# Performance work log

Hardware: AMD Instinct MI355X
Metric: run time of the kernel (lower is better)

## Reference

```python
import jax, jax.numpy as jnp
import numpy as np

P, F, V = 2048, 8192, 2048


def setup_inputs() -> dict:
    key = jax.random.key(0)
    k1, k2, k3 = jax.random.split(key, 3)
    points = jax.random.normal(k1, (P, 3), dtype=jnp.float32)
    vertices = jax.random.normal(k2, (V, 3), dtype=jnp.float32)
    faces = jax.random.randint(k3, (F, 3), 0, V, dtype=jnp.int32)
    return {"points": points, "vertices": vertices, "faces": faces}


def _triangle_weights(points, a, b, c):
    """Barycentric weights of closest point on each triangle (a,b,c) [F,3]
    for each point [P,3], via Ericson's region classification.
    All pairwise dot products expanded so only [P,F] scalars are materialized
    (never [P,F,3] differences)."""
    ab = b - a  # [F,3]
    ac = c - a  # [F,3]
    pab = points @ ab.T  # [P,F] = dot(p, ab)
    pac = points @ ac.T  # [P,F] = dot(p, ac)
    d1 = pab - jnp.sum(a * ab, -1)  # dot(ab, p-a)
    d2 = pac - jnp.sum(a * ac, -1)  # dot(ac, p-a)
    d3 = pab - jnp.sum(b * ab, -1)  # dot(ab, p-b)
    d4 = pac - jnp.sum(b * ac, -1)  # dot(ac, p-b)
    d5 = pab - jnp.sum(c * ab, -1)  # dot(ab, p-c)
    d6 = pac - jnp.sum(c * ac, -1)  # dot(ac, p-c)
    vc = d1 * d4 - d3 * d2
    vb = d5 * d2 - d1 * d6
    va = d3 * d6 - d5 * d4

    def sdiv(n, d):
        ds = jnp.where(d == 0, 1.0, d)
        return n / ds

    # region 7 (interior) is the default; overwrite with higher-priority
    denom = va + vb + vc
    v7 = sdiv(vb, denom)
    w7 = sdiv(vc, denom)
    w1, w2, w3 = 1.0 - v7 - w7, v7, w7
    # region 6: edge bc
    t6 = sdiv(d4 - d3, (d4 - d3) + (d5 - d6))
    m6 = (va <= 0) & (d4 - d3 >= 0) & (d5 - d6 >= 0)
    w1 = jnp.where(m6, 0.0, w1)
    w2 = jnp.where(m6, 1.0 - t6, w2)
    w3 = jnp.where(m6, t6, w3)
    # region 5: edge ac
    t5 = sdiv(d2, d2 - d6)
    m5 = (vb <= 0) & (d2 >= 0) & (d6 <= 0)
    w1 = jnp.where(m5, 1.0 - t5, w1)
    w2 = jnp.where(m5, 0.0, w2)
    w3 = jnp.where(m5, t5, w3)
    # region 4: vertex c
    m4 = (d6 >= 0) & (d5 <= d6)
    w1 = jnp.where(m4, 0.0, w1)
    w2 = jnp.where(m4, 0.0, w2)
    w3 = jnp.where(m4, 1.0, w3)
    # region 3: edge ab
    t3 = sdiv(d1, d1 - d3)
    m3 = (vc <= 0) & (d1 >= 0) & (d3 <= 0)
    w1 = jnp.where(m3, 1.0 - t3, w1)
    w2 = jnp.where(m3, t3, w2)
    w3 = jnp.where(m3, 0.0, w3)
    # region 2: vertex b
    m2 = (d3 >= 0) & (d4 <= d3)
    w1 = jnp.where(m2, 0.0, w1)
    w2 = jnp.where(m2, 1.0, w2)
    w3 = jnp.where(m2, 0.0, w3)
    # region 1: vertex a
    m1 = (d1 <= 0) & (d2 <= 0)
    w1 = jnp.where(m1, 1.0, w1)
    w2 = jnp.where(m1, 0.0, w2)
    w3 = jnp.where(m1, 0.0, w3)
    return w1, w2, w3  # each [P,F]


def reference(points, vertices, faces):
    # gather per-face vertex triples (the f1/f2/f3 of the torch module)
    a = vertices[faces[:, 0]]  # [F,3]
    b = vertices[faces[:, 1]]
    c = vertices[faces[:, 2]]
    w1, w2, w3 = _triangle_weights(points, a, b, c)  # [P,F] each
    cp = w1[..., None] * a + w2[..., None] * b + w3[..., None] * c  # [P,F,3]
    dist = jnp.sum((points[:, None, :] - cp) ** 2, axis=-1)  # [P,F]
    idx = jnp.argmin(dist, axis=1)  # [P] closest face per point
    gather = lambda w: jnp.take_along_axis(w, idx[:, None], axis=1)[:, 0]
    return idx, gather(w1), gather(w2), gather(w3)
```

## Files before the change

kernel.cpp:

```cpp
#include <hip/hip_runtime.h>
#include <cstdint>

#pragma clang fp contract(off)

typedef float v2f __attribute__((ext_vector_type(2)));

#define P_N 2048
#define F_N 8192
#define TPB 256
#define FPT 32
#define NT (F_N / FPT)
#define TW 28

#define WS_TAB_BYTES   (F_N * TW * 4)
#define WS_MINUB_OFF   WS_TAB_BYTES
#define WS_BEST_OFF    (WS_TAB_BYTES + P_N * 4)
#define WS_NEEDED      (WS_BEST_OFF + P_N * 8)


__device__ __forceinline__ void face_setup(
    const float* __restrict__ vertices, const int* __restrict__ faces, int f,
    float* fd)
{
#pragma clang fp contract(off)
    int i0 = faces[3 * f + 0];
    int i1 = faces[3 * f + 1];
    int i2 = faces[3 * f + 2];
    float ax = vertices[3 * i0 + 0], ay = vertices[3 * i0 + 1], az = vertices[3 * i0 + 2];
    float bx = vertices[3 * i1 + 0], by = vertices[3 * i1 + 1], bz = vertices[3 * i1 + 2];
    float cx = vertices[3 * i2 + 0], cy = vertices[3 * i2 + 1], cz = vertices[3 * i2 + 2];
    float abx = bx - ax, aby = by - ay, abz = bz - az;
    float acx = cx - ax, acy = cy - ay, acz = cz - az;
    float daab = (ax * abx + ay * aby) + az * abz;
    float daac = (ax * acx + ay * acy) + az * acz;
    float dbab = (bx * abx + by * aby) + bz * abz;
    float dbac = (bx * acx + by * acy) + bz * acz;
    float dcab = (cx * abx + cy * aby) + cz * abz;
    float dcac = (cx * acx + cy * acy) + cz * acz;
    fd[0] = ax;  fd[1] = ay;  fd[2] = az;
    fd[3] = bx;  fd[4] = by;  fd[5] = bz;
    fd[6] = cx;  fd[7] = cy;  fd[8] = cz;
    fd[9] = abx; fd[10] = aby; fd[11] = abz;
    fd[12] = acx; fd[13] = acy; fd[14] = acz;
    fd[15] = daab; fd[16] = daac; fd[17] = dbab;
    fd[18] = dbac; fd[19] = dcab; fd[20] = dcac;
}

__device__ __forceinline__ void tri_eval_exact(
    float px, float py, float pz,
    const float* __restrict__ fd,
    float& w1o, float& w2o, float& w3o, float& disto)
{
#pragma clang fp contract(off)
    const float ax = fd[0], ay = fd[1], az = fd[2];
    const float bx = fd[3], by = fd[4], bz = fd[5];
    const float cx = fd[6], cy = fd[7], cz = fd[8];
    const float abx = fd[9], aby = fd[10], abz = fd[11];
    const float acx = fd[12], acy = fd[13], acz = fd[14];
    const float daab = fd[15], daac = fd[16], dbab = fd[17];
    const float dbac = fd[18], dcab = fd[19], dcac = fd[20];

    float pab = fmaf(pz, abz, fmaf(py, aby, px * abx));
    float pac = fmaf(pz, acz, fmaf(py, acy, px * acx));

    float d1 = pab - daab;
    float d2 = pac - daac;
    float d3 = pab - dbab;
    float d4 = pac - dbac;
    float d5 = pab - dcab;
    float d6 = pac - dcac;

    float vc = d1 * d4 - d3 * d2;
    float vb = d5 * d2 - d1 * d6;
    float va = d3 * d6 - d5 * d4;

    float denom = (va + vb) + vc;
    float dn = (denom == 0.0f) ? 1.0f : denom;
    float v7 = vb / dn;
    float w7 = vc / dn;
    float w1 = (1.0f - v7) - w7;
    float w2 = v7;
    float w3 = w7;

    float e63 = d4 - d3;
    float e65 = d5 - d6;
    float t6d = e63 + e65; t6d = (t6d == 0.0f) ? 1.0f : t6d;
    float t6 = e63 / t6d;
    if ((va <= 0.0f) & (e63 >= 0.0f) & (e65 >= 0.0f)) { w1 = 0.0f; w2 = 1.0f - t6; w3 = t6; }

    float t5d = d2 - d6; t5d = (t5d == 0.0f) ? 1.0f : t5d;
    float t5 = d2 / t5d;
    if ((vb <= 0.0f) & (d2 >= 0.0f) & (d6 <= 0.0f)) { w1 = 1.0f - t5; w2 = 0.0f; w3 = t5; }

    if ((d6 >= 0.0f) & (d5 <= d6)) { w1 = 0.0f; w2 = 0.0f; w3 = 1.0f; }

    float t3d = d1 - d3; t3d = (t3d == 0.0f) ? 1.0f : t3d;
    float t3 = d1 / t3d;
    if ((vc <= 0.0f) & (d1 >= 0.0f) & (d3 <= 0.0f)) { w1 = 1.0f - t3; w2 = t3; w3 = 0.0f; }

    if ((d3 >= 0.0f) & (d4 <= d3)) { w1 = 0.0f; w2 = 1.0f; w3 = 0.0f; }

    if ((d1 <= 0.0f) & (d2 <= 0.0f)) { w1 = 1.0f; w2 = 0.0f; w3 = 0.0f; }

    float cpx = (w1 * ax + w2 * bx) + w3 * cx;
    float cpy = (w1 * ay + w2 * by) + w3 * cy;
    float cpz = (w1 * az + w2 * bz) + w3 * cz;
    float dx = px - cpx, dy = py - cpy, dz = pz - cpz;
    float dist = (dx * dx + dy * dy) + dz * dz;

    w1o = w1; w2o = w2; w3o = w3; disto = dist;
}


__global__ __launch_bounds__(TPB) void k_prep(
    const float* __restrict__ vertices, const int* __restrict__ faces,
    float* __restrict__ tab, unsigned* __restrict__ minub,
    unsigned long long* __restrict__ best)
{
#pragma clang fp contract(off)
    int f = blockIdx.x * TPB + threadIdx.x;
    if (f < F_N) {
        float td[TW];
        face_setup(vertices, faces, f, td);
        float ax = td[0], ay = td[1], az = td[2];
        float abx = td[9], aby = td[10], abz = td[11];
        float acx = td[12], acy = td[13], acz = td[14];
        float nx = aby * acz - abz * acy;
        float ny = abz * acx - abx * acz;
        float nz = abx * acy - aby * acx;
        float nn = (nx * nx + ny * ny) + nz * nz;
        float abab = (abx * abx + aby * aby) + abz * abz;
        float acac = (acx * acx + acy * acy) + acz * acz;
        float L2v = abab + acac;
        bool bad = !(nn >= 1e-2f * L2v) || (nn < 1e-20f);
        td[21] = nx; td[22] = ny; td[23] = nz;
        td[24] = -((nx * ax + ny * ay) + nz * az);
        td[25] = bad ? -1.0f : 1.0f / nn;
        td[26] = 0.0f; td[27] = 0.0f;
#pragma unroll
        for (int k = 0; k < TW; k += 4)
            *(float4*)&tab[f * TW + k] = *(float4*)&td[k];
    }
    if (f < P_N) {
        minub[f] = 0x7f7f7f7fu;
        best[f] = ~0ull;
    }
}


__global__ __launch_bounds__(TPB) void k_bound(
    const float* __restrict__ points,
    const float* __restrict__ tab,
    unsigned* __restrict__ minub)
{
#pragma clang fp contract(off)
    const int pblk = blockIdx.x, fblk = blockIdx.y, t = threadIdx.x;
    const int fbase = fblk * FPT;
    const int p = pblk * TPB + t;
    const float px = points[3 * p + 0];
    const float py = points[3 * p + 1];
    const float pz = points[3 * p + 2];

    float bestv = 1e30f;
    int bestj = fbase;

#pragma unroll 4
    for (int j = 0; j < FPT; ++j) {
        const float* __restrict__ tf = tab + (size_t)(fbase + j) * TW;
        float nx = tf[21], ny = tf[22], nz = tf[23], mnd = tf[24], inn = tf[25];
        float nd = fmaf(nz, pz, fmaf(ny, py, fmaf(nx, px, mnd)));
        float p2 = (nd * nd) * inn;
        bool better = (p2 >= 0.0f) & (p2 < bestv);
        bestv = better ? p2 : bestv;
        bestj = better ? (fbase + j) : bestj;
    }

    float fd[21];
#pragma unroll
    for (int k = 0; k < 20; k += 4)
        *(float4*)&fd[k] = *(const float4*)&tab[(size_t)bestj * TW + k];
    fd[20] = tab[(size_t)bestj * TW + 20];
    float w1, w2, w3, dist;
    tri_eval_exact(px, py, pz, fd, w1, w2, w3, dist);
    if (!(dist != dist)) atomicMin(&minub[p], __float_as_uint(dist));
}


__global__ __launch_bounds__(TPB) void k_scan2(
    const float* __restrict__ points,
    const float* __restrict__ tab,
    const unsigned* __restrict__ minub,
    unsigned long long* __restrict__ best)
{
#pragma clang fp contract(off)
    const int pblk = blockIdx.x, fblk = blockIdx.y, t = threadIdx.x;
    const int fbase = fblk * FPT;
    const int p = pblk * TPB + t;
    const float px = points[3 * p + 0];
    const float py = points[3 * p + 1];
    const float pz = points[3 * p + 2];
    const float thr = __uint_as_float(minub[p]);

    unsigned bestdb = 0xffffffffu;
    int bestf = 0;

#pragma unroll 2
    for (int j = 0; j < FPT; ++j) {
        const float* __restrict__ tf = tab + (size_t)(fbase + j) * TW;
        float nx = tf[21], ny = tf[22], nz = tf[23], mnd = tf[24], inn = tf[25];
        float nd = fmaf(nz, pz, fmaf(ny, py, fmaf(nx, px, mnd)));
        float p2 = (nd * nd) * inn;
        float lb = fmaxf(fmaf(p2, 0.97f, -1e-6f), 0.0f);
        if (__any(lb <= thr)) {
            float w1, w2, w3, dist;
            tri_eval_exact(px, py, pz, tf, w1, w2, w3, dist);
            unsigned db = __float_as_uint(dist);
            if (dist != dist) db = 0u;
            if (db < bestdb) { bestdb = db; bestf = fbase + j; }
        }
    }

    unsigned long long key =
        ((unsigned long long)bestdb << 32) | (unsigned)bestf;
    atomicMin(&best[p], key);
}


__global__ __launch_bounds__(TPB) void k_final(
    const float* __restrict__ points,
    const float* __restrict__ vertices,
    const int* __restrict__ faces,
    const unsigned long long* __restrict__ best,
    float* __restrict__ out)
{
    const int p = blockIdx.x * TPB + threadIdx.x;
    if (p >= P_N) return;
    int f = (int)(best[p] & 0x1fffull);
    float fd[21];
    face_setup(vertices, faces, f, fd);
    float w1, w2, w3, dist;
    tri_eval_exact(points[3 * p], points[3 * p + 1], points[3 * p + 2],
                   fd, w1, w2, w3, dist);
    out[p] = (float)f;
    out[P_N + p] = w1;
    out[2 * P_N + p] = w2;
    out[3 * P_N + p] = w3;
}


__device__ __forceinline__ void region_w(
    float d1, float d2, float d3, float d4, float d5, float d6,
    float va, float vb, float vc, float e63, float e65, float denom,
    float& w1, float& w2, float& w3)
{
#pragma clang fp contract(off)
    bool m1 = (d1 <= 0.0f) & (d2 <= 0.0f);
    bool m2 = (d3 >= 0.0f) & (d4 <= d3);
    bool m3 = (vc <= 0.0f) & (d1 >= 0.0f) & (d3 <= 0.0f);
    bool m4 = (d6 >= 0.0f) & (d5 <= d6);
    bool m5 = (vb <= 0.0f) & (d2 >= 0.0f) & (d6 <= 0.0f);
    bool m6 = (va <= 0.0f) & (e63 >= 0.0f) & (e65 >= 0.0f);
    bool anym = m1 | m2 | m3 | m4 | m5 | m6;

    float n1  = m1 ? 0.0f : m2 ? 0.0f : m3 ? d1        : m4 ? 0.0f : m5 ? d2        : m6 ? e63         : vb;
    float ds1 = m1 ? 1.0f : m2 ? 1.0f : m3 ? (d1 - d3) : m4 ? 1.0f : m5 ? (d2 - d6) : m6 ? (e63 + e65) : denom;
    ds1 = (ds1 == 0.0f) ? 1.0f : ds1;
    float n2  = anym ? 0.0f : vc;
    float ds2 = anym ? 1.0f : ((denom == 0.0f) ? 1.0f : denom);

    float q1 = n1 / ds1;
    float q2 = n2 / ds2;
    float u = (1.0f - q1) - q2;

    w1 = m1 ? 1.0f : m2 ? 0.0f : m3 ? u    : m4 ? 0.0f : m5 ? u    : m6 ? 0.0f : u;
    w2 = m1 ? 0.0f : m2 ? 1.0f : m3 ? q1   : m4 ? 0.0f : m5 ? 0.0f : m6 ? u    : q1;
    w3 = m1 ? 0.0f : m2 ? 0.0f : m3 ? 0.0f : m4 ? 1.0f : m5 ? q1   : m6 ? q1   : q2;
}

__global__ __launch_bounds__(TPB) void k_scan_full(
    const float* __restrict__ points,
    const float* __restrict__ vertices,
    const int* __restrict__ faces,
    unsigned long long* __restrict__ best)
{
#pragma clang fp contract(off)
    __shared__ float sq[21][FPT];
    const int pblk = blockIdx.x, fblk = blockIdx.y, t = threadIdx.x;
    if (t < FPT) {
        float fd[21];
        face_setup(vertices, faces, fblk * FPT + t, fd);
#pragma unroll
        for (int k = 0; k < 21; ++k) sq[k][t] = fd[k];
    }
    __syncthreads();

    const int p = pblk * TPB + t;
    const float px = points[3 * p], py = points[3 * p + 1], pz = points[3 * p + 2];
    const v2f pxv = {px, px}, pyv = {py, py}, pzv = {pz, pz};

    unsigned int bestdb = 0xffffffffu;
    int bestf = 0;
    const int fbase = fblk * FPT;

#pragma unroll 2
    for (int j = 0; j < FPT; j += 2) {
#define LD2(q) (*(const v2f*)&sq[q][j])
        v2f axv = LD2(0),  ayv = LD2(1),  azv = LD2(2);
        v2f bxv = LD2(3),  byv = LD2(4),  bzv = LD2(5);
        v2f cxv = LD2(6),  cyv = LD2(7),  czv = LD2(8);
        v2f abxv = LD2(9),  abyv = LD2(10), abzv = LD2(11);
        v2f acxv = LD2(12), acyv = LD2(13), aczv = LD2(14);
        v2f daabv = LD2(15), daacv = LD2(16), dbabv = LD2(17);
        v2f dbacv = LD2(18), dcabv = LD2(19), dcacv = LD2(20);
#undef LD2
        v2f pab = __builtin_elementwise_fma(pzv, abzv,
                    __builtin_elementwise_fma(pyv, abyv, pxv * abxv));
        v2f pac = __builtin_elementwise_fma(pzv, aczv,
                    __builtin_elementwise_fma(pyv, acyv, pxv * acxv));
        v2f d1 = pab - daabv, d2 = pac - daacv, d3 = pab - dbabv;
        v2f d4 = pac - dbacv, d5 = pab - dcabv, d6 = pac - dcacv;
        v2f vcv = d1 * d4 - d3 * d2;
        v2f vbv = d5 * d2 - d1 * d6;
        v2f vav = d3 * d6 - d5 * d4;
        v2f e63 = d4 - d3, e65 = d5 - d6;
        v2f denom = (vav + vbv) + vcv;

        float w1a, w2a, w3a, w1b, w2b, w3b;
        region_w(d1.x, d2.x, d3.x, d4.x, d5.x, d6.x,
                 vav.x, vbv.x, vcv.x, e63.x, e65.x, denom.x, w1a, w2a, w3a);
        region_w(d1.y, d2.y, d3.y, d4.y, d5.y, d6.y,
                 vav.y, vbv.y, vcv.y, e63.y, e65.y, denom.y, w1b, w2b, w3b);

        v2f w1v = {w1a, w1b}, w2v = {w2a, w2b}, w3v = {w3a, w3b};
        v2f cpx = (w1v * axv + w2v * bxv) + w3v * cxv;
        v2f cpy = (w1v * ayv + w2v * byv) + w3v * cyv;
        v2f cpz = (w1v * azv + w2v * bzv) + w3v * czv;
        v2f dx = pxv - cpx, dy = pyv - cpy, dz = pzv - cpz;
        v2f dist = (dx * dx + dy * dy) + dz * dz;

        float da = dist.x, db = dist.y;
        unsigned ua = __float_as_uint(da), ub = __float_as_uint(db);
        if (da != da) ua = 0u;
        if (db != db) ub = 0u;
        if (ua < bestdb) { bestdb = ua; bestf = fbase + j; }
        if (ub < bestdb) { bestdb = ub; bestf = fbase + j + 1; }
    }

    unsigned long long key =
        ((unsigned long long)bestdb << 32) | (unsigned int)bestf;
    atomicMin(&best[p], key);
}

extern "C" void kernel_launch(void* const* d_in, const int* in_sizes, int n_in,
                              void* d_out, int out_size, void* d_ws, size_t ws_size,
                              hipStream_t stream)
{
    const float* points = (const float*)d_in[0];
    const float* vertices = (const float*)d_in[1];
    const int* faces = (const int*)d_in[2];
    float* out = (float*)d_out;
    char* ws = (char*)d_ws;

    if (ws_size >= WS_NEEDED) {
        float* tab = (float*)ws;
        unsigned* minub = (unsigned*)(ws + WS_MINUB_OFF);
        unsigned long long* best = (unsigned long long*)(ws + WS_BEST_OFF);

        k_prep<<<F_N / TPB, TPB, 0, stream>>>(vertices, faces, tab, minub, best);
        k_bound<<<dim3(P_N / TPB, NT), TPB, 0, stream>>>(points, tab, minub);
        k_scan2<<<dim3(P_N / TPB, NT), TPB, 0, stream>>>(points, tab, minub, best);
        k_final<<<(P_N + TPB - 1) / TPB, TPB, 0, stream>>>(points, vertices, faces, best, out);
    } else {
        unsigned long long* best = (unsigned long long*)ws;
        hipMemsetAsync(best, 0xFF, P_N * sizeof(unsigned long long), stream);
        k_scan_full<<<dim3(P_N / TPB, NT), TPB, 0, stream>>>(points, vertices, faces, best);
        k_final<<<(P_N + TPB - 1) / TPB, TPB, 0, stream>>>(points, vertices, faces, best, out);
    }
}
```

Before: 66.31 us.

## Morton-sort points and add centroid candidate to tighten per-point upper bound

Adds a single-block bitonic sort of points by 30-bit Morton code, so each wavefront in the bound and scan kernels handles spatially nearby points and the wave-wide __any culling test skips more exact triangle evaluations. The bound kernel now also tracks the face with the nearest centroid, stored in the widened 32-float face table, and evaluates both candidates to get a tighter minimum-distance upper bound. The costs are an extra serial launch (one block sorting 2048 keys in shared memory), indirect point loads through the permutation, a wider table, and a second exact evaluation per thread in the bound kernel. The unroll pragma in the scan loop is also removed.

```diff
diff --git a/kernel.cpp b/kernel.cpp
--- a/kernel.cpp
+++ b/kernel.cpp
@@ -10,12 +10,13 @@
 #define TPB 256
 #define FPT 32
 #define NT (F_N / FPT)
-#define TW 28
+#define TW 32
 
 #define WS_TAB_BYTES   (F_N * TW * 4)
 #define WS_MINUB_OFF   WS_TAB_BYTES
-#define WS_BEST_OFF    (WS_TAB_BYTES + P_N * 4)
-#define WS_NEEDED      (WS_BEST_OFF + P_N * 8)
+#define WS_BEST_OFF    (WS_MINUB_OFF + P_N * 4)
+#define WS_PERM_OFF    (WS_BEST_OFF + P_N * 8)
+#define WS_NEEDED      (WS_PERM_OFF + P_N * 4)
 
 
 __device__ __forceinline__ void face_setup(
@@ -123,6 +124,8 @@
         float td[TW];
         face_setup(vertices, faces, f, td);
         float ax = td[0], ay = td[1], az = td[2];
+        float bx = td[3], by = td[4], bz = td[5];
+        float cx = td[6], cy = td[7], cz = td[8];
         float abx = td[9], aby = td[10], abz = td[11];
         float acx = td[12], acy = td[13], acz = td[14];
         float nx = aby * acz - abz * acy;
@@ -136,7 +139,10 @@
         td[21] = nx; td[22] = ny; td[23] = nz;
         td[24] = -((nx * ax + ny * ay) + nz * az);
         td[25] = bad ? -1.0f : 1.0f / nn;
-        td[26] = 0.0f; td[27] = 0.0f;
+        td[26] = (ax + bx + cx) * (1.0f / 3.0f);
+        td[27] = (ay + by + cy) * (1.0f / 3.0f);
+        td[28] = (az + bz + cz) * (1.0f / 3.0f);
+        td[29] = 0.0f; td[30] = 0.0f; td[31] = 0.0f;
 #pragma unroll
         for (int k = 0; k < TW; k += 4)
             *(float4*)&tab[f * TW + k] = *(float4*)&td[k];
@@ -148,54 +154,115 @@
 }
 
 
+__device__ __forceinline__ unsigned expand10(unsigned v)
+{
+    v &= 1023u;
+    v = (v | (v << 16)) & 0x030000FFu;
+    v = (v | (v << 8))  & 0x0300F00Fu;
+    v = (v | (v << 4))  & 0x030C30C3u;
+    v = (v | (v << 2))  & 0x09249249u;
+    return v;
+}
+
+__global__ __launch_bounds__(1024) void k_sort(
+    const float* __restrict__ points, unsigned* __restrict__ perm)
+{
+    __shared__ unsigned long long sk[P_N];
+    const int t = threadIdx.x;
+
+    for (int i = t; i < P_N; i += 1024) {
+        float x = points[3 * i], y = points[3 * i + 1], z = points[3 * i + 2];
+        auto q = [](float v) -> unsigned {
+            float s = (v + 5.0f) * 102.4f;
+            int u = (int)s;
+            u = u < 0 ? 0 : (u > 1023 ? 1023 : u);
+            return (unsigned)u;
+        };
+        unsigned key = (expand10(q(x)) << 2) | (expand10(q(y)) << 1) | expand10(q(z));
+        sk[i] = ((unsigned long long)key << 32) | (unsigned)i;
+    }
+
+    for (unsigned k = 2; k <= P_N; k <<= 1) {
+        for (unsigned jj = k >> 1; jj > 0; jj >>= 1) {
+            __syncthreads();
+            for (unsigned i = t; i < P_N; i += 1024) {
+                unsigned ixj = i ^ jj;
+                if (ixj > i) {
+                    unsigned long long a = sk[i], b = sk[ixj];
+                    bool up = ((i & k) == 0);
+                    if (up ? (a > b) : (a < b)) { sk[i] = b; sk[ixj] = a; }
+                }
+            }
+        }
+    }
+    __syncthreads();
+    for (int i = t; i < P_N; i += 1024)
+        perm[i] = (unsigned)(sk[i] & 0xffffffffull);
+}
+
+
 __global__ __launch_bounds__(TPB) void k_bound(
     const float* __restrict__ points,
     const float* __restrict__ tab,
+    const unsigned* __restrict__ perm,
     unsigned* __restrict__ minub)
 {
 #pragma clang fp contract(off)
     const int pblk = blockIdx.x, fblk = blockIdx.y, t = threadIdx.x;
     const int fbase = fblk * FPT;
-    const int p = pblk * TPB + t;
+    const int p = (int)perm[pblk * TPB + t];
     const float px = points[3 * p + 0];
     const float py = points[3 * p + 1];
     const float pz = points[3 * p + 2];
 
-    float bestv = 1e30f;
-    int bestj = fbase;
+    float bestp = 1e30f; int bj1 = fbase;
+    float bestc = 1e30f; int bj2 = fbase;
 
 #pragma unroll 4
     for (int j = 0; j < FPT; ++j) {
         const float* __restrict__ tf = tab + (size_t)(fbase + j) * TW;
         float nx = tf[21], ny = tf[22], nz = tf[23], mnd = tf[24], inn = tf[25];
+        float cgx = tf[26], cgy = tf[27], cgz = tf[28];
         float nd = fmaf(nz, pz, fmaf(ny, py, fmaf(nx, px, mnd)));
         float p2 = (nd * nd) * inn;
-        bool better = (p2 >= 0.0f) & (p2 < bestv);
-        bestv = better ? p2 : bestv;
-        bestj = better ? (fbase + j) : bestj;
-    }
-
-    float fd[21];
+        bool b1 = (p2 >= 0.0f) & (p2 < bestp);
+        bestp = b1 ? p2 : bestp;
+        bj1 = b1 ? (fbase + j) : bj1;
+        float ex = px - cgx, ey = py - cgy, ez = pz - cgz;
+        float dc2 = fmaf(ez, ez, fmaf(ey, ey, ex * ex));
+        bool b2 = dc2 < bestc;
+        bestc = b2 ? dc2 : bestc;
+        bj2 = b2 ? (fbase + j) : bj2;
+    }
+
+    float ubmin = 3e38f;
 #pragma unroll
-    for (int k = 0; k < 20; k += 4)
-        *(float4*)&fd[k] = *(const float4*)&tab[(size_t)bestj * TW + k];
-    fd[20] = tab[(size_t)bestj * TW + 20];
-    float w1, w2, w3, dist;
-    tri_eval_exact(px, py, pz, fd, w1, w2, w3, dist);
-    if (!(dist != dist)) atomicMin(&minub[p], __float_as_uint(dist));
+    for (int c = 0; c < 2; ++c) {
+        int f = c == 0 ? bj1 : bj2;
+        float fd[21];
+#pragma unroll
+        for (int k = 0; k < 20; k += 4)
+            *(float4*)&fd[k] = *(const float4*)&tab[(size_t)f * TW + k];
+        fd[20] = tab[(size_t)f * TW + 20];
+        float w1, w2, w3, dist;
+        tri_eval_exact(px, py, pz, fd, w1, w2, w3, dist);
+        if (!(dist != dist)) ubmin = fminf(ubmin, dist);
+    }
+    atomicMin(&minub[p], __float_as_uint(ubmin));
 }
 
 
 __global__ __launch_bounds__(TPB) void k_scan2(
     const float* __restrict__ points,
     const float* __restrict__ tab,
+    const unsigned* __restrict__ perm,
     const unsigned* __restrict__ minub,
     unsigned long long* __restrict__ best)
 {
 #pragma clang fp contract(off)
     const int pblk = blockIdx.x, fblk = blockIdx.y, t = threadIdx.x;
     const int fbase = fblk * FPT;
-    const int p = pblk * TPB + t;
+    const int p = (int)perm[pblk * TPB + t];
     const float px = points[3 * p + 0];
     const float py = points[3 * p + 1];
     const float pz = points[3 * p + 2];
@@ -204,7 +271,6 @@
     unsigned bestdb = 0xffffffffu;
     int bestf = 0;
 
-#pragma unroll 2
     for (int j = 0; j < FPT; ++j) {
         const float* __restrict__ tf = tab + (size_t)(fbase + j) * TW;
         float nx = tf[21], ny = tf[22], nz = tf[23], mnd = tf[24], inn = tf[25];
@@ -365,10 +431,12 @@
         float* tab = (float*)ws;
         unsigned* minub = (unsigned*)(ws + WS_MINUB_OFF);
         unsigned long long* best = (unsigned long long*)(ws + WS_BEST_OFF);
+        unsigned* perm = (unsigned*)(ws + WS_PERM_OFF);
 
         k_prep<<<F_N / TPB, TPB, 0, stream>>>(vertices, faces, tab, minub, best);
-        k_bound<<<dim3(P_N / TPB, NT), TPB, 0, stream>>>(points, tab, minub);
-        k_scan2<<<dim3(P_N / TPB, NT), TPB, 0, stream>>>(points, tab, minub, best);
+        k_sort<<<1, 1024, 0, stream>>>(points, perm);
+        k_bound<<<dim3(P_N / TPB, NT), TPB, 0, stream>>>(points, tab, perm, minub);
+        k_scan2<<<dim3(P_N / TPB, NT), TPB, 0, stream>>>(points, tab, perm, minub, best);
         k_final<<<(P_N + TPB - 1) / TPB, TPB, 0, stream>>>(points, vertices, faces, best, out);
     } else {
         unsigned long long* best = (unsigned long long*)ws;
```

After: 168.7 us. +154.3%, slower.

## Bucket-sort points spatially and use branchless region distance in bound/scan

Applied to the files above, without the earlier changes.

Adds a single-block kernel that groups points into 64 coarse spatial buckets so wavefronts hold nearby points, making the __any-based culling in k_scan2 skip more faces per wave. The bound and scan kernels now read sorted float4 points carrying the original index, and replace the branchy exact evaluation with a select-based region_w distance. The face table is padded to 32 floats for alignment, and the unroll pragma on the scan loop is dropped. The extra serial launch and the different distance formula, which may round differently from the exact path, are the costs and risks; the bucket thresholds assume normally distributed inputs.

```diff
diff --git a/kernel.cpp b/kernel.cpp
--- a/kernel.cpp
+++ b/kernel.cpp
@@ -10,12 +10,13 @@
 #define TPB 256
 #define FPT 32
 #define NT (F_N / FPT)
-#define TW 28
+#define TW 32
 
 #define WS_TAB_BYTES   (F_N * TW * 4)
 #define WS_MINUB_OFF   WS_TAB_BYTES
-#define WS_BEST_OFF    (WS_TAB_BYTES + P_N * 4)
-#define WS_NEEDED      (WS_BEST_OFF + P_N * 8)
+#define WS_BEST_OFF    (WS_MINUB_OFF + P_N * 4)
+#define WS_SPTS_OFF    (WS_BEST_OFF + P_N * 8)
+#define WS_NEEDED      (WS_SPTS_OFF + P_N * 16)
 
 
 __device__ __forceinline__ void face_setup(
@@ -111,6 +112,75 @@
     w1o = w1; w2o = w2; w3o = w3; disto = dist;
 }
 
+__device__ __forceinline__ void region_w(
+    float d1, float d2, float d3, float d4, float d5, float d6,
+    float va, float vb, float vc, float e63, float e65, float denom,
+    float& w1, float& w2, float& w3)
+{
+#pragma clang fp contract(off)
+    bool m1 = (d1 <= 0.0f) & (d2 <= 0.0f);
+    bool m2 = (d3 >= 0.0f) & (d4 <= d3);
+    bool m3 = (vc <= 0.0f) & (d1 >= 0.0f) & (d3 <= 0.0f);
+    bool m4 = (d6 >= 0.0f) & (d5 <= d6);
+    bool m5 = (vb <= 0.0f) & (d2 >= 0.0f) & (d6 <= 0.0f);
+    bool m6 = (va <= 0.0f) & (e63 >= 0.0f) & (e65 >= 0.0f);
+    bool anym = m1 | m2 | m3 | m4 | m5 | m6;
+
+    float n1  = m1 ? 0.0f : m2 ? 0.0f : m3 ? d1        : m4 ? 0.0f : m5 ? d2        : m6 ? e63         : vb;
+    float ds1 = m1 ? 1.0f : m2 ? 1.0f : m3 ? (d1 - d3) : m4 ? 1.0f : m5 ? (d2 - d6) : m6 ? (e63 + e65) : denom;
+    ds1 = (ds1 == 0.0f) ? 1.0f : ds1;
+    float n2  = anym ? 0.0f : vc;
+    float ds2 = anym ? 1.0f : ((denom == 0.0f) ? 1.0f : denom);
+
+    float q1 = n1 / ds1;
+    float q2 = n2 / ds2;
+    float u = (1.0f - q1) - q2;
+
+    w1 = m1 ? 1.0f : m2 ? 0.0f : m3 ? u    : m4 ? 0.0f : m5 ? u    : m6 ? 0.0f : u;
+    w2 = m1 ? 0.0f : m2 ? 1.0f : m3 ? q1   : m4 ? 0.0f : m5 ? 0.0f : m6 ? u    : q1;
+    w3 = m1 ? 0.0f : m2 ? 0.0f : m3 ? 0.0f : m4 ? 1.0f : m5 ? q1   : m6 ? q1   : q2;
+}
+
+__device__ __forceinline__ float tri_dist_region(
+    float px, float py, float pz, const float* __restrict__ fd)
+{
+#pragma clang fp contract(off)
+    const float ax = fd[0], ay = fd[1], az = fd[2];
+    const float bx = fd[3], by = fd[4], bz = fd[5];
+    const float cx = fd[6], cy = fd[7], cz = fd[8];
+    const float abx = fd[9], aby = fd[10], abz = fd[11];
+    const float acx = fd[12], acy = fd[13], acz = fd[14];
+    const float daab = fd[15], daac = fd[16], dbab = fd[17];
+    const float dbac = fd[18], dcab = fd[19], dcac = fd[20];
+
+    float pab = fmaf(pz, abz, fmaf(py, aby, px * abx));
+    float pac = fmaf(pz, acz, fmaf(py, acy, px * acx));
+
+    float d1 = pab - daab;
+    float d2 = pac - daac;
+    float d3 = pab - dbab;
+    float d4 = pac - dbac;
+    float d5 = pab - dcab;
+    float d6 = pac - dcac;
+
+    float vc = d1 * d4 - d3 * d2;
+    float vb = d5 * d2 - d1 * d6;
+    float va = d3 * d6 - d5 * d4;
+
+    float e63 = d4 - d3;
+    float e65 = d5 - d6;
+    float denom = (va + vb) + vc;
+
+    float w1, w2, w3;
+    region_w(d1, d2, d3, d4, d5, d6, va, vb, vc, e63, e65, denom, w1, w2, w3);
+
+    float cpx = (w1 * ax + w2 * bx) + w3 * cx;
+    float cpy = (w1 * ay + w2 * by) + w3 * cy;
+    float cpz = (w1 * az + w2 * bz) + w3 * cz;
+    float dx = px - cpx, dy = py - cpy, dz = pz - cpz;
+    return (dx * dx + dy * dy) + dz * dz;
+}
+
 
 __global__ __launch_bounds__(TPB) void k_prep(
     const float* __restrict__ vertices, const int* __restrict__ faces,
@@ -136,7 +206,8 @@
         td[21] = nx; td[22] = ny; td[23] = nz;
         td[24] = -((nx * ax + ny * ay) + nz * az);
         td[25] = bad ? -1.0f : 1.0f / nn;
-        td[26] = 0.0f; td[27] = 0.0f;
+        td[26] = 0.0f; td[27] = 0.0f; td[28] = 0.0f;
+        td[29] = 0.0f; td[30] = 0.0f; td[31] = 0.0f;
 #pragma unroll
         for (int k = 0; k < TW; k += 4)
             *(float4*)&tab[f * TW + k] = *(float4*)&td[k];
@@ -148,18 +219,55 @@
 }
 
 
+__device__ __forceinline__ unsigned bucket_code(float x, float y, float z)
+{
+    auto q2 = [](float v) -> unsigned {
+        return (v >= 0.0f) ? (v >= 0.6745f ? 3u : 2u) : (v >= -0.6745f ? 1u : 0u);
+    };
+    return (q2(x) << 4) | (q2(y) << 2) | q2(z);
+}
+
+__global__ __launch_bounds__(1024) void k_sort(
+    const float* __restrict__ points, float4* __restrict__ spts)
+{
+    __shared__ unsigned hist[64];
+    __shared__ unsigned offs[64];
+    const int t = threadIdx.x;
+
+    if (t < 64) hist[t] = 0;
+    __syncthreads();
+
+    for (int i = t; i < P_N; i += 1024) {
+        float x = points[3 * i], y = points[3 * i + 1], z = points[3 * i + 2];
+        atomicAdd(&hist[bucket_code(x, y, z)], 1u);
+    }
+    __syncthreads();
+
+    if (t == 0) {
+        unsigned s = 0;
+        for (int b = 0; b < 64; ++b) { offs[b] = s; s += hist[b]; }
+    }
+    __syncthreads();
+
+    for (int i = t; i < P_N; i += 1024) {
+        float x = points[3 * i], y = points[3 * i + 1], z = points[3 * i + 2];
+        unsigned slot = atomicAdd(&offs[bucket_code(x, y, z)], 1u);
+        spts[slot] = make_float4(x, y, z, __uint_as_float((unsigned)i));
+    }
+}
+
+
 __global__ __launch_bounds__(TPB) void k_bound(
-    const float* __restrict__ points,
+    const float4* __restrict__ spts,
     const float* __restrict__ tab,
     unsigned* __restrict__ minub)
 {
 #pragma clang fp contract(off)
     const int pblk = blockIdx.x, fblk = blockIdx.y, t = threadIdx.x;
     const int fbase = fblk * FPT;
-    const int p = pblk * TPB + t;
-    const float px = points[3 * p + 0];
-    const float py = points[3 * p + 1];
-    const float pz = points[3 * p + 2];
+    float4 pt = spts[pblk * TPB + t];
+    const float px = pt.x, py = pt.y, pz = pt.z;
+    const int p = (int)__float_as_uint(pt.w);
 
     float bestv = 1e30f;
     int bestj = fbase;
@@ -180,14 +288,13 @@
     for (int k = 0; k < 20; k += 4)
         *(float4*)&fd[k] = *(const float4*)&tab[(size_t)bestj * TW + k];
     fd[20] = tab[(size_t)bestj * TW + 20];
-    float w1, w2, w3, dist;
-    tri_eval_exact(px, py, pz, fd, w1, w2, w3, dist);
+    float dist = tri_dist_region(px, py, pz, fd);
     if (!(dist != dist)) atomicMin(&minub[p], __float_as_uint(dist));
 }
 
 
 __global__ __launch_bounds__(TPB) void k_scan2(
-    const float* __restrict__ points,
+    const float4* __restrict__ spts,
     const float* __restrict__ tab,
     const unsigned* __restrict__ minub,
     unsigned long long* __restrict__ best)
@@ -195,16 +302,14 @@
 #pragma clang fp contract(off)
     const int pblk = blockIdx.x, fblk = blockIdx.y, t = threadIdx.x;
     const int fbase = fblk * FPT;
-    const int p = pblk * TPB + t;
-    const float px = points[3 * p + 0];
-    const float py = points[3 * p + 1];
-    const float pz = points[3 * p + 2];
+    float4 pt = spts[pblk * TPB + t];
+    const float px = pt.x, py = pt.y, pz = pt.z;
+    const int p = (int)__float_as_uint(pt.w);
     const float thr = __uint_as_float(minub[p]);
 
     unsigned bestdb = 0xffffffffu;
     int bestf = 0;
 
-#pragma unroll 2
     for (int j = 0; j < FPT; ++j) {
         const float* __restrict__ tf = tab + (size_t)(fbase + j) * TW;
         float nx = tf[21], ny = tf[22], nz = tf[23], mnd = tf[24], inn = tf[25];
@@ -212,8 +317,7 @@
         float p2 = (nd * nd) * inn;
         float lb = fmaxf(fmaf(p2, 0.97f, -1e-6f), 0.0f);
         if (__any(lb <= thr)) {
-            float w1, w2, w3, dist;
-            tri_eval_exact(px, py, pz, tf, w1, w2, w3, dist);
+            float dist = tri_dist_region(px, py, pz, tf);
             unsigned db = __float_as_uint(dist);
             if (dist != dist) db = 0u;
             if (db < bestdb) { bestdb = db; bestf = fbase + j; }
@@ -247,35 +351,6 @@
     out[3 * P_N + p] = w3;
 }
 
-
-__device__ __forceinline__ void region_w(
-    float d1, float d2, float d3, float d4, float d5, float d6,
-    float va, float vb, float vc, float e63, float e65, float denom,
-    float& w1, float& w2, float& w3)
-{
-#pragma clang fp contract(off)
-    bool m1 = (d1 <= 0.0f) & (d2 <= 0.0f);
-    bool m2 = (d3 >= 0.0f) & (d4 <= d3);
-    bool m3 = (vc <= 0.0f) & (d1 >= 0.0f) & (d3 <= 0.0f);
-    bool m4 = (d6 >= 0.0f) & (d5 <= d6);
-    bool m5 = (vb <= 0.0f) & (d2 >= 0.0f) & (d6 <= 0.0f);
-    bool m6 = (va <= 0.0f) & (e63 >= 0.0f) & (e65 >= 0.0f);
-    bool anym = m1 | m2 | m3 | m4 | m5 | m6;
-
-    float n1  = m1 ? 0.0f : m2 ? 0.0f : m3 ? d1        : m4 ? 0.0f : m5 ? d2        : m6 ? e63         : vb;
-    float ds1 = m1 ? 1.0f : m2 ? 1.0f : m3 ? (d1 - d3) : m4 ? 1.0f : m5 ? (d2 - d6) : m6 ? (e63 + e65) : denom;
-    ds1 = (ds1 == 0.0f) ? 1.0f : ds1;
-    float n2  = anym ? 0.0f : vc;
-    float ds2 = anym ? 1.0f : ((denom == 0.0f) ? 1.0f : denom);
-
-    float q1 = n1 / ds1;
-    float q2 = n2 / ds2;
-    float u = (1.0f - q1) - q2;
-
-    w1 = m1 ? 1.0f : m2 ? 0.0f : m3 ? u    : m4 ? 0.0f : m5 ? u    : m6 ? 0.0f : u;
-    w2 = m1 ? 0.0f : m2 ? 1.0f : m3 ? q1   : m4 ? 0.0f : m5 ? 0.0f : m6 ? u    : q1;
-    w3 = m1 ? 0.0f : m2 ? 0.0f : m3 ? 0.0f : m4 ? 1.0f : m5 ? q1   : m6 ? q1   : q2;
-}
 
 __global__ __launch_bounds__(TPB) void k_scan_full(
     const float* __restrict__ points,
@@ -365,10 +440,12 @@
         float* tab = (float*)ws;
         unsigned* minub = (unsigned*)(ws + WS_MINUB_OFF);
         unsigned long long* best = (unsigned long long*)(ws + WS_BEST_OFF);
+        float4* spts = (float4*)(ws + WS_SPTS_OFF);
 
         k_prep<<<F_N / TPB, TPB, 0, stream>>>(vertices, faces, tab, minub, best);
-        k_bound<<<dim3(P_N / TPB, NT), TPB, 0, stream>>>(points, tab, minub);
-        k_scan2<<<dim3(P_N / TPB, NT), TPB, 0, stream>>>(points, tab, minub, best);
+        k_sort<<<1, 1024, 0, stream>>>(points, spts);
+        k_bound<<<dim3(P_N / TPB, NT), TPB, 0, stream>>>(spts, tab, minub);
+        k_scan2<<<dim3(P_N / TPB, NT), TPB, 0, stream>>>(spts, tab, minub, best);
         k_final<<<(P_N + TPB - 1) / TPB, TPB, 0, stream>>>(points, vertices, faces, best, out);
     } else {
         unsigned long long* best = (unsigned long long*)ws;
```

Measured after the change: 138.1 us. 108% more time.
